# Performance work log

Hardware: AMD Instinct MI355X
Metric: run time of the kernel (lower is better)

## Reference

```python
import jax, jax.numpy as jnp
import numpy as np

BATCH = 16384
NUM_IN = 4096
NUM_OUT = 1024
NNZ = 262144
BN_EPS = 1e-3  # keras BatchNormalization default epsilon


def setup_inputs() -> dict:
    key = jax.random.key(0)
    ks = jax.random.split(key, 6)
    x = jax.random.normal(ks[0], (BATCH, NUM_IN), dtype=jnp.float32)
    sp_values = jax.random.normal(ks[1], (NNZ,), dtype=jnp.float32)
    gamma = jnp.ones((NUM_IN,), dtype=jnp.float32)
    beta = jnp.zeros((NUM_IN,), dtype=jnp.float32)
    moving_mean = jax.random.normal(ks[2], (NUM_IN,), dtype=jnp.float32)
    # positive moving variance in [0.5, 1.5)
    moving_var = jax.random.uniform(ks[3], (NUM_IN,), dtype=jnp.float32, minval=0.5, maxval=1.5)
    sp_rows = jax.random.randint(ks[4], (NNZ,), 0, NUM_IN, dtype=jnp.int32)
    sp_cols = jax.random.randint(ks[5], (NNZ,), 0, NUM_OUT, dtype=jnp.int32)
    return {
        "x": x,
        "sp_values": sp_values,
        "gamma": gamma,
        "beta": beta,
        "moving_mean": moving_mean,
        "moving_var": moving_var,
        "sp_rows": sp_rows,
        "sp_cols": sp_cols,
    }


def reference(x, sp_values, gamma, beta, moving_mean, moving_var, sp_rows, sp_cols):
    # BatchNorm (inference mode, moving statistics), fused elementwise
    h = (x - moving_mean) * (gamma * jax.lax.rsqrt(moving_var + BN_EPS)) + beta
    # Scatter the fixed-index sparse weights into a small dense [NUM_IN, NUM_OUT]
    # matrix (16 MB), then a single dense GEMM — honors SparseTensor semantics
    # (duplicate indices accumulate) while staying GEMM-efficient.
    W = jnp.zeros((NUM_IN, NUM_OUT), dtype=x.dtype).at[sp_rows, sp_cols].add(sp_values)
    return h @ W  # [BATCH, NUM_OUT]
```

## Files before the change

### kernel.cpp

```cpp
#include <hip/hip_runtime.h>
#include <hip/hip_bf16.h>

#define BATCH   16384
#define NUM_IN  4096
#define NUM_OUT 1024
#define NNZ     262144
#define BN_EPS  1e-3f

typedef __attribute__((ext_vector_type(8)))  short short8;
typedef __attribute__((ext_vector_type(4)))  float f32x4;
typedef __attribute__((ext_vector_type(4)))  unsigned int u32x4;

typedef __attribute__((address_space(3))) void        lds_void_t;
typedef const __attribute__((address_space(1))) void  g_void_t;

__device__ inline unsigned short f2bf(float f) {
    unsigned int u = __builtin_bit_cast(unsigned int, f);
    u += 0x7fffu + ((u >> 16) & 1u);
    return (unsigned short)(u >> 16);
}

__global__ void k_zero(f32x4* __restrict__ p) {
    p[(size_t)blockIdx.x * 256 + threadIdx.x] = f32x4{0.f, 0.f, 0.f, 0.f};
}

__global__ void k_scatter(const float* __restrict__ v, const int* __restrict__ r,
                          const int* __restrict__ c, float* __restrict__ wtf) {
    int i = blockIdx.x * 256 + threadIdx.x;
    atomicAdd(&wtf[(size_t)c[i] * NUM_IN + r[i]], v[i]);
}

__global__ void k_wprep(const float* __restrict__ wtf, const float* __restrict__ gamma,
                        const float* __restrict__ beta, const float* __restrict__ mean,
                        const float* __restrict__ var, unsigned short* __restrict__ wtb,
                        float* __restrict__ bias) {
    const int n = blockIdx.x;
    const int t = threadIdx.x;
    float acc = 0.f;
    for (int k = t; k < NUM_IN; k += 256) {
        float w = wtf[(size_t)n * NUM_IN + k];
        float s = gamma[k] * rsqrtf(var[k] + BN_EPS);
        wtb[(size_t)n * NUM_IN + k] = f2bf(w * s);
        acc += (beta[k] - mean[k] * s) * w;
    }
    #pragma unroll
    for (int o = 32; o; o >>= 1) acc += __shfl_down(acc, o, 64);
    __shared__ float red[4];
    if ((t & 63) == 0) red[t >> 6] = acc;
    __syncthreads();
    if (t == 0) bias[n] = red[0] + red[1] + red[2] + red[3];
}

#define BM 256
#define BN 256
#define BK 64
#define NT (NUM_IN / BK)
#define SLOT 65536
#define BOFF 32768

__global__ __launch_bounds__(512, 2) void k_gemm(const float* __restrict__ x,
                                                 const unsigned short* __restrict__ wt,
                                                 const float* __restrict__ bias,
                                                 float* __restrict__ out) {
    __shared__ __align__(128) char lds[2 * SLOT];

    const int bid = blockIdx.x;
    const int swz = (bid & 7) * 32 + (bid >> 3);
    const int m0 = (swz >> 2) * BM;
    const int n0 = (swz & 3) * BN;

    const int t    = threadIdx.x;
    const int lane = t & 63;
    const int wid  = t >> 6;
    const int wm   = wid >> 2;
    const int wn   = wid & 3;

    const char* xb = (const char*)x;
    const char* wb = (const char*)wt;

    const int awBase = ((t >> 2) & 1) * 16384 + (t >> 7) * 1024
                     + (((((t >> 3) & 15) | ((t & 3) << 4)) ^ (t & 7)) * 16);
    const int la0 = (lane ^ (lane >> 4)) * 16;
    const int la1 = (lane ^ ((lane >> 4) | 4)) * 16;
    const int bColB = (wn * 64 + (lane & 15)) * 128;
    const int bC0   = (((lane >> 4)    ) ^ (lane & 7)) * 16;
    const int bC1   = ((4 + (lane >> 4)) ^ (lane & 7)) * 16;

    f32x4 rA[8];
    auto loadA = [&](int kt) {
        #pragma unroll
        for (int i = 0; i < 4; ++i) {
            const char* p = xb + (size_t)(m0 + i * 64 + (t >> 3)) * (NUM_IN * 4)
                          + (size_t)kt * (BK * 4) + (t & 7) * 32;
            rA[2 * i]     = *(const f32x4*)(p);
            rA[2 * i + 1] = *(const f32x4*)(p + 16);
        }
    };
    auto convWriteA = [&](int sl) {
        char* dst = lds + sl * SLOT + awBase;
        #pragma unroll
        for (int i = 0; i < 4; ++i) {
            const unsigned int* f0 = (const unsigned int*)&rA[2 * i];
            const unsigned int* f1 = (const unsigned int*)&rA[2 * i + 1];
            u32x4 w;
            w[0] = __builtin_amdgcn_perm(f0[1], f0[0], 0x07060302u);
            w[1] = __builtin_amdgcn_perm(f0[3], f0[2], 0x07060302u);
            w[2] = __builtin_amdgcn_perm(f1[1], f1[0], 0x07060302u);
            w[3] = __builtin_amdgcn_perm(f1[3], f1[2], 0x07060302u);
            *(u32x4*)(dst + i * 4096) = w;
        }
    };
    auto stageB = [&](int kt, int sl) {
        #pragma unroll
        for (int i = 0; i < 4; ++i) {
            int col = i * 64 + (t >> 3);
            size_t src = (size_t)(n0 + col) * (NUM_IN * 2) + (size_t)kt * (BK * 2)
                       + (((t & 7) ^ ((t >> 3) & 7)) * 16);
            __builtin_amdgcn_global_load_lds((g_void_t*)(wb + src),
                (lds_void_t*)(lds + sl * SLOT + BOFF + i * 8192 + t * 16), 16, 0, 0);
        }
    };

    short8 af[4], bf0[4], bf1[4];
    auto readA4 = [&](const char* A, int kk, int mh) {
        const char* base = A + kk * 16384 + (wm * 8 + mh * 4) * 1024
                         + (kk ? la1 : la0);
        af[0] = *(const short8*)(base);
        af[1] = *(const short8*)(base + 1024);
        af[2] = *(const short8*)(base + 2048);
        af[3] = *(const short8*)(base + 3072);
    };
    auto readB4 = [&](const char* B, int co, short8* bf) {
        const char* base = B + bColB + co;
        bf[0] = *(const short8*)(base);
        bf[1] = *(const short8*)(base + 2048);
        bf[2] = *(const short8*)(base + 4096);
        bf[3] = *(const short8*)(base + 6144);
    };

    f32x4 acc[8][4] = {};
    auto mfma16 = [&](short8* bf, int mlb) {
        __builtin_amdgcn_s_setprio(1);
        #pragma unroll
        for (int mi = 0; mi < 4; ++mi)
            #pragma unroll
            for (int nf = 0; nf < 4; ++nf)
                acc[mlb + mi][nf] = __builtin_amdgcn_mfma_f32_16x16x32_bf16(
                    af[mi], bf[nf], acc[mlb + mi][nf], 0, 0, 0);
        __builtin_amdgcn_s_setprio(0);
    };

    loadA(0);
    stageB(0, 0);
    stageB(1, 1);
    asm volatile("s_waitcnt vmcnt(8)" ::: "memory");
    convWriteA(0);
    asm volatile("s_waitcnt vmcnt(4)" ::: "memory");
    asm volatile("s_waitcnt lgkmcnt(0)" ::: "memory");
    __builtin_amdgcn_s_barrier();

    #pragma unroll 1
    for (int kt = 0; kt < NT; ++kt) {
        const int s = kt & 1;
        const char* Ap = lds + s * SLOT;
        const char* Bp = Ap + BOFF;
        const bool st1 = (kt + 1) < NT;
        const bool st2 = (kt + 2) < NT;
        if (st1) loadA(kt + 1);
        readB4(Bp, bC0, bf0);
        readA4(Ap, 0, 0);
        __builtin_amdgcn_s_barrier();
        asm volatile("s_waitcnt lgkmcnt(0)" ::: "memory");
        __builtin_amdgcn_sched_barrier(0);
        mfma16(bf0, 0);
        __builtin_amdgcn_s_barrier();
        readA4(Ap, 0, 1);
        __builtin_amdgcn_s_barrier();
        asm volatile("s_waitcnt lgkmcnt(0)" ::: "memory");
        __builtin_amdgcn_sched_barrier(0);
        mfma16(bf0, 4);
        __builtin_amdgcn_s_barrier();
        readB4(Bp, bC1, bf1);
        readA4(Ap, 1, 0);
        __builtin_amdgcn_s_barrier();
        asm volatile("s_waitcnt lgkmcnt(0)" ::: "memory");
        __builtin_amdgcn_sched_barrier(0);
        mfma16(bf1, 0);
        __builtin_amdgcn_s_barrier();
        if (st2) stageB(kt + 2, s);
        readA4(Ap, 1, 1);
        if (st1) {
            if (st2) asm volatile("s_waitcnt vmcnt(4)" ::: "memory");
            else     asm volatile("s_waitcnt vmcnt(0)" ::: "memory");
            convWriteA(s ^ 1);
        }
        __builtin_amdgcn_s_barrier();
        asm volatile("s_waitcnt lgkmcnt(0)" ::: "memory");
        __builtin_amdgcn_sched_barrier(0);
        mfma16(bf1, 4);
        __builtin_amdgcn_s_barrier();
    }

    float bj[4];
    #pragma unroll
    for (int n = 0; n < 4; ++n) bj[n] = bias[n0 + wn * 64 + n * 16 + (lane & 15)];
    const int mb = m0 + wm * 128 + (lane >> 4) * 4;
    const int nb = n0 + wn * 64 + (lane & 15);
    #pragma unroll
    for (int ml = 0; ml < 8; ++ml)
        #pragma unroll
        for (int n = 0; n < 4; ++n)
            #pragma unroll
            for (int r = 0; r < 4; ++r)
                out[(size_t)(mb + ml * 16 + r) * NUM_OUT + (nb + n * 16)] =
                    acc[ml][n][r] + bj[n];
}

extern "C" void kernel_launch(void* const* d_in, const int* in_sizes, int n_in,
                              void* d_out, int out_size, void* d_ws, size_t ws_size,
                              hipStream_t stream) {
    const float* x     = (const float*)d_in[0];
    const float* spv   = (const float*)d_in[1];
    const float* gamma = (const float*)d_in[2];
    const float* beta  = (const float*)d_in[3];
    const float* mean  = (const float*)d_in[4];
    const float* var   = (const float*)d_in[5];
    const int*   rows  = (const int*)d_in[6];
    const int*   cols  = (const int*)d_in[7];
    float* out = (float*)d_out;

    float* wtf = (float*)d_out;
    unsigned short* wtb = (unsigned short*)d_ws;
    float* bias = (float*)((char*)d_ws + (size_t)NUM_IN * NUM_OUT * sizeof(unsigned short));

    hipLaunchKernelGGL(k_zero, dim3((NUM_IN * NUM_OUT / 4) / 256), dim3(256), 0, stream,
                       (f32x4*)wtf);
    hipLaunchKernelGGL(k_scatter, dim3(NNZ / 256), dim3(256), 0, stream,
                       spv, rows, cols, wtf);
    hipLaunchKernelGGL(k_wprep, dim3(NUM_OUT), dim3(256), 0, stream,
                       wtf, gamma, beta, mean, var, wtb, bias);
    hipLaunchKernelGGL(k_gemm, dim3((BATCH / BM) * (NUM_OUT / BN)), dim3(512), 0, stream,
                       x, wtb, bias, out);
}
```

Before: 214.3 us.

## Split A prefetch into halves and restage B one tile ahead

Splits the fp32 A-tile global load and its bf16 conversion/LDS write into two halves, spread across the MFMA phases of each k-iteration. B is now staged only one tile ahead into the other buffer slot, instead of two. The aim is to lower peak register use for A staging and spread global loads and conversions more evenly between compute blocks. In exchange, B's prefetch distance shrinks and a full vmcnt(0) wait at the top of each iteration may expose memory latency.

```diff
diff --git a/kernel.cpp b/kernel.cpp
--- a/kernel.cpp
+++ b/kernel.cpp
@@ -86,28 +86,51 @@
     const int bC0   = (((lane >> 4)    ) ^ (lane & 7)) * 16;
     const int bC1   = ((4 + (lane >> 4)) ^ (lane & 7)) * 16;
 
-    f32x4 rA[8];
-    auto loadA = [&](int kt) {
-        #pragma unroll
-        for (int i = 0; i < 4; ++i) {
+    f32x4 rc0[4], rc1[4];
+    auto loadA01 = [&](int kt) {
+        #pragma unroll
+        for (int i = 0; i < 2; ++i) {
             const char* p = xb + (size_t)(m0 + i * 64 + (t >> 3)) * (NUM_IN * 4)
                           + (size_t)kt * (BK * 4) + (t & 7) * 32;
-            rA[2 * i]     = *(const f32x4*)(p);
-            rA[2 * i + 1] = *(const f32x4*)(p + 16);
-        }
-    };
-    auto convWriteA = [&](int sl) {
+            rc0[2 * i]     = *(const f32x4*)(p);
+            rc0[2 * i + 1] = *(const f32x4*)(p + 16);
+        }
+    };
+    auto loadA23 = [&](int kt) {
+        #pragma unroll
+        for (int i = 0; i < 2; ++i) {
+            const char* p = xb + (size_t)(m0 + (i + 2) * 64 + (t >> 3)) * (NUM_IN * 4)
+                          + (size_t)kt * (BK * 4) + (t & 7) * 32;
+            rc1[2 * i]     = *(const f32x4*)(p);
+            rc1[2 * i + 1] = *(const f32x4*)(p + 16);
+        }
+    };
+    auto convWriteA01 = [&](int sl) {
         char* dst = lds + sl * SLOT + awBase;
         #pragma unroll
-        for (int i = 0; i < 4; ++i) {
-            const unsigned int* f0 = (const unsigned int*)&rA[2 * i];
-            const unsigned int* f1 = (const unsigned int*)&rA[2 * i + 1];
+        for (int i = 0; i < 2; ++i) {
+            const unsigned int* f0 = (const unsigned int*)&rc0[2 * i];
+            const unsigned int* f1 = (const unsigned int*)&rc0[2 * i + 1];
             u32x4 w;
             w[0] = __builtin_amdgcn_perm(f0[1], f0[0], 0x07060302u);
             w[1] = __builtin_amdgcn_perm(f0[3], f0[2], 0x07060302u);
             w[2] = __builtin_amdgcn_perm(f1[1], f1[0], 0x07060302u);
             w[3] = __builtin_amdgcn_perm(f1[3], f1[2], 0x07060302u);
             *(u32x4*)(dst + i * 4096) = w;
+        }
+    };
+    auto convWriteA23 = [&](int sl) {
+        char* dst = lds + sl * SLOT + awBase;
+        #pragma unroll
+        for (int i = 0; i < 2; ++i) {
+            const unsigned int* f0 = (const unsigned int*)&rc1[2 * i];
+            const unsigned int* f1 = (const unsigned int*)&rc1[2 * i + 1];
+            u32x4 w;
+            w[0] = __builtin_amdgcn_perm(f0[1], f0[0], 0x07060302u);
+            w[1] = __builtin_amdgcn_perm(f0[3], f0[2], 0x07060302u);
+            w[2] = __builtin_amdgcn_perm(f1[1], f1[0], 0x07060302u);
+            w[3] = __builtin_amdgcn_perm(f1[3], f1[2], 0x07060302u);
+            *(u32x4*)(dst + (i + 2) * 4096) = w;
         }
     };
     auto stageB = [&](int kt, int sl) {
@@ -150,12 +173,10 @@
         __builtin_amdgcn_s_setprio(0);
     };
 
-    loadA(0);
+    loadA01(0); loadA23(0);
     stageB(0, 0);
-    stageB(1, 1);
-    asm volatile("s_waitcnt vmcnt(8)" ::: "memory");
-    convWriteA(0);
     asm volatile("s_waitcnt vmcnt(4)" ::: "memory");
+    convWriteA01(0); convWriteA23(0);
     asm volatile("s_waitcnt lgkmcnt(0)" ::: "memory");
     __builtin_amdgcn_s_barrier();
 
@@ -164,9 +185,9 @@
         const int s = kt & 1;
         const char* Ap = lds + s * SLOT;
         const char* Bp = Ap + BOFF;
-        const bool st1 = (kt + 1) < NT;
-        const bool st2 = (kt + 2) < NT;
-        if (st1) loadA(kt + 1);
+        const bool st = (kt + 1) < NT;
+        asm volatile("s_waitcnt vmcnt(0)" ::: "memory");
+        if (st) loadA01(kt + 1);
         readB4(Bp, bC0, bf0);
         readA4(Ap, 0, 0);
         __builtin_amdgcn_s_barrier();
@@ -174,12 +195,17 @@
         __builtin_amdgcn_sched_barrier(0);
         mfma16(bf0, 0);
         __builtin_amdgcn_s_barrier();
+        if (st) { loadA23(kt + 1); stageB(kt + 1, s ^ 1); }
         readA4(Ap, 0, 1);
         __builtin_amdgcn_s_barrier();
         asm volatile("s_waitcnt lgkmcnt(0)" ::: "memory");
         __builtin_amdgcn_sched_barrier(0);
         mfma16(bf0, 4);
         __builtin_amdgcn_s_barrier();
+        if (st) {
+            asm volatile("s_waitcnt vmcnt(8)" ::: "memory");
+            convWriteA01(s ^ 1);
+        }
         readB4(Bp, bC1, bf1);
         readA4(Ap, 1, 0);
         __builtin_amdgcn_s_barrier();
@@ -187,13 +213,11 @@
         __builtin_amdgcn_sched_barrier(0);
         mfma16(bf1, 0);
         __builtin_amdgcn_s_barrier();
-        if (st2) stageB(kt + 2, s);
+        if (st) {
+            asm volatile("s_waitcnt vmcnt(4)" ::: "memory");
+            convWriteA23(s ^ 1);
+        }
         readA4(Ap, 1, 1);
-        if (st1) {
-            if (st2) asm volatile("s_waitcnt vmcnt(4)" ::: "memory");
-            else     asm volatile("s_waitcnt vmcnt(0)" ::: "memory");
-            convWriteA(s ^ 1);
-        }
         __builtin_amdgcn_s_barrier();
         asm volatile("s_waitcnt lgkmcnt(0)" ::: "memory");
         __builtin_amdgcn_sched_barrier(0);
```

New measurement: 215.3 us. Within noise of the previous version (+0.5%).
